# Performance work log

Hardware: AMD Instinct MI355X
Metric: run time of the kernel (lower is better)

## Reference

```python
import jax, jax.numpy as jnp
import numpy as np

N, E, G, S = 200000, 800000, 2048, 128
NUM_OPS, NUM_ETYPES, NUMERIC = 64, 4, 12
H, TEXT, VOCAB, OUT = 256, 64, 30000, 512
IN0 = 32 + NUMERIC  # 44


def _ln(h, eps=1e-5):
    # nn.LayerNorm with default (ones/zeros) affine, created fresh each forward
    m = h.mean(-1, keepdims=True)
    v = ((h - m) ** 2).mean(-1, keepdims=True)
    return (h - m) * jax.lax.rsqrt(v + eps)


def _leaky(v):
    return jnp.where(v > 0, v, 0.1 * v)  # LeakyReLU(0.1)


def setup_inputs() -> dict:
    key = jax.random.key(0)
    ks = jax.random.split(key, 40)
    x = jax.random.normal(ks[0], (N, 1 + NUMERIC), jnp.float32)
    x = x.at[:, 0].set(jax.random.randint(ks[1], (N,), 0, NUM_OPS).astype(jnp.float32))
    inp = {
        'x': x,
        'edge_index': jax.random.randint(ks[2], (2, E), 0, N),
        'edge_attr': jax.random.randint(ks[3], (E,), 0, NUM_ETYPES),
        'batch': jnp.sort(jax.random.randint(ks[4], (N,), 0, G)),
        'sql_ids': jax.random.randint(ks[5], (G, S), 0, VOCAB),
        'sql_mask': (jax.random.uniform(ks[6], (G, S)) > 0.3).astype(jnp.float32),
        'op_embed': jax.random.normal(ks[7], (NUM_OPS, 32), jnp.float32),
        'edge_embed': jax.random.normal(ks[8], (NUM_ETYPES, 16), jnp.float32),
        'token_embed': jax.random.normal(ks[9], (VOCAB, TEXT), jnp.float32).at[0].set(0.0),  # padding_idx=0
    }
    dims = [IN0, H, H]
    k = 10
    for i, d in enumerate(dims):
        inp[f'lin_w{i}'] = jax.random.normal(ks[k], (d, 16), jnp.float32) * 0.05; k += 1
        inp[f'lin_b{i}'] = jnp.zeros((d,), jnp.float32)
        inp[f'eps{i}'] = jnp.zeros((), jnp.float32)  # train_eps init 0
        inp[f'W1_{i}'] = jax.random.normal(ks[k], (H, d), jnp.float32) * 0.05; k += 1
        inp[f'b1_{i}'] = jnp.zeros((H,), jnp.float32)
        inp[f'W2_{i}'] = jax.random.normal(ks[k], (H, H), jnp.float32) * 0.05; k += 1
        inp[f'b2_{i}'] = jnp.zeros((H,), jnp.float32)
    inp['mW1'] = jax.random.normal(ks[k], (H, H + 3 + TEXT), jnp.float32) * 0.05; k += 1
    inp['mb1'] = jnp.zeros((H,), jnp.float32)
    inp['mW2'] = jax.random.normal(ks[k], (OUT, H), jnp.float32) * 0.05
    inp['mb2'] = jnp.zeros((OUT,), jnp.float32)
    return inp


def reference(x, edge_index, edge_attr, batch, sql_ids, sql_mask,
              op_embed, edge_embed, token_embed,
              lin_w0, lin_b0, eps0, W1_0, b1_0, W2_0, b2_0,
              lin_w1, lin_b1, eps1, W1_1, b1_1, W2_1, b2_1,
              lin_w2, lin_b2, eps2, W1_2, b1_2, W2_2, b2_2,
              mW1, mb1, mW2, mb2):
    op_ids = jnp.clip(x[:, 0].astype(jnp.int32), 0, NUM_OPS - 1)
    nums = x[:, 1:]
    e_idx = jnp.minimum(edge_attr, NUM_ETYPES - 1)  # clamp_max
    edge_emb = edge_embed[e_idx]                    # [E,16]
    h = jnp.concatenate([op_embed[op_ids], nums], 1)  # [N,44]
    src, dst = edge_index[0], edge_index[1]
    convs = [(lin_w0, lin_b0, eps0, W1_0, b1_0, W2_0, b2_0),
             (lin_w1, lin_b1, eps1, W1_1, b1_1, W2_1, b2_1),
             (lin_w2, lin_b2, eps2, W1_2, b1_2, W2_2, b2_2)]
    for (lw, lb, eps, W1, b1, W2, b2) in convs:
        h_in = h
        # GINEConv: msg = relu(x_j + Lin(edge_attr)); sum-aggregate at dst
        msg = jax.nn.relu(h[src] + edge_emb @ lw.T + lb)        # [E,d]
        aggr = jax.ops.segment_sum(msg, dst, num_segments=h.shape[0])
        z = (1.0 + eps) * h + aggr
        h = jax.nn.relu(z @ W1.T + b1) @ W2.T + b2              # conv MLP -> [N,H]
        h = _ln(h)
        h = _leaky(h + h_in) if h_in.shape[-1] == h.shape[-1] else _leaky(h)
    # graph pooling
    g = jax.ops.segment_sum(h, batch, num_segments=G)            # global_add_pool
    count = jax.ops.segment_sum(jnp.ones((h.shape[0],), h.dtype), batch, num_segments=G)
    denom = jnp.maximum(count, 1.0)                              # scatter_mean semantics
    fanout_mean = jax.ops.segment_sum(x[:, 5], batch, num_segments=G) / denom
    cost_mean = jax.ops.segment_sum(x[:, 4], batch, num_segments=G) / denom
    graph_sum = jnp.stack([count, fanout_mean, cost_mean], 1)    # [G,3]
    # text pooling (masked mean)
    emb = token_embed[sql_ids]                                   # [G,S,TEXT]
    summed = (emb * sql_mask[..., None]).sum(1)
    lengths = jnp.maximum(sql_mask.sum(1, keepdims=True), 1.0)
    text_feat = summed / lengths
    cat = jnp.concatenate([g, graph_sum, text_feat], 1)          # [G, H+3+TEXT]
    hid = _leaky(cat @ mW1.T + mb1)                              # Dropout(0.1) is identity in eval
    return hid @ mW2.T + mb2                                     # [G, OUT]
```

## Files before the change

kernel.cpp:

```cpp
#include <hip/hip_runtime.h>

#define NN 200000
#define EE 800000
#define GG 2048
#define NBLK ((NN + 255) / 256)

typedef __attribute__((ext_vector_type(8))) short short8;
typedef __attribute__((ext_vector_type(4))) float f32x4;

__device__ __forceinline__ float bf2f(ushort u){
  unsigned x = ((unsigned)u) << 16;
  return __uint_as_float(x);
}
__device__ __forceinline__ ushort f2bf(float f){
  unsigned x = __float_as_uint(f);
  x += 0x7fffu + ((x >> 16) & 1u);
  return (ushort)(x >> 16);
}

__device__ __forceinline__ void swz256(const float* __restrict__ W, ushort* __restrict__ o, int idx){
  int ks = idx >> 13, rem = idx & 8191;
  int j16 = rem >> 9, rem2 = rem & 511;
  int ln = rem2 >> 3, t = rem2 & 7;
  int row = j16*16 + (ln & 15);
  int k = ks*32 + (ln >> 4)*8 + t;
  o[idx] = f2bf(W[(size_t)row*256 + k]);
}

__global__ __launch_bounds__(256) void prep_k(
    const float* __restrict__ W10, const float* __restrict__ W20,
    const float* __restrict__ W11, const float* __restrict__ W21,
    const float* __restrict__ W12, const float* __restrict__ W22,
    const float* __restrict__ lw0, const float* __restrict__ lb0,
    const float* __restrict__ lw1, const float* __restrict__ lb1,
    const float* __restrict__ lw2, const float* __restrict__ lb2,
    const float* __restrict__ eE, const float* __restrict__ mW1,
    const float* __restrict__ mW2,
    ushort* __restrict__ wb10, ushort* __restrict__ wb20,
    ushort* __restrict__ wb11, ushort* __restrict__ wb21,
    ushort* __restrict__ wb12, ushort* __restrict__ wb22,
    ushort* __restrict__ mW1b, ushort* __restrict__ mW2b,
    float* __restrict__ eb)
{
  int b = blockIdx.x, tid = threadIdx.x;
  if (b < 64){
    int idx = b*256 + tid;
    int ks = idx >> 13, rem = idx & 8191;
    int j16 = rem >> 9, rem2 = rem & 511;
    int ln = rem2 >> 3, t = rem2 & 7;
    int row = j16*16 + (ln & 15);
    int k = ks*32 + (ln >> 4)*8 + t;
    wb10[idx] = (k < 44) ? f2bf(W10[row*44 + k]) : (ushort)0;
    return;
  }
  b -= 64;
  if (b < 256){ swz256(W20, wb20, b*256+tid); return; } b -= 256;
  if (b < 256){ swz256(W11, wb11, b*256+tid); return; } b -= 256;
  if (b < 256){ swz256(W21, wb21, b*256+tid); return; } b -= 256;
  if (b < 256){ swz256(W12, wb12, b*256+tid); return; } b -= 256;
  if (b < 256){ swz256(W22, wb22, b*256+tid); return; } b -= 256;
  if (b < 384){
    int idx = b*256 + tid; int o = idx / 384, k = idx - o*384;
    mW1b[idx] = (k < 323) ? f2bf(mW1[(size_t)o*323 + k]) : (ushort)0;
    return;
  }
  b -= 384;
  if (b < 512){ int idx = b*256+tid; mW2b[idx] = f2bf(mW2[idx]); return; } b -= 512;
  int li = b >> 2, t = b & 3;
  const float* lw = (li == 0) ? lw0 : ((li == 1) ? lw1 : lw2);
  const float* lb = (li == 0) ? lb0 : ((li == 1) ? lb1 : lb2);
  int d = (li == 0) ? 44 : 256;
  float v = 0.f;
  if (tid < d){
    float a = 0.f;
    #pragma unroll
    for (int j = 0; j < 16; j++) a += eE[t*16 + j] * lw[tid*16 + j];
    v = a + lb[tid];
  }
  eb[(li*4 + t)*256 + tid] = v;
}

__global__ __launch_bounds__(256) void build_h0_k(
    const float* __restrict__ x, const float* __restrict__ opE, ushort* __restrict__ h0)
{
  int idx = blockIdx.x*256 + threadIdx.x;
  int i = idx >> 6, c = idx & 63;
  float v = 0.f;
  if (c < 32){
    int op = (int)x[(size_t)i*13];
    op = op < 0 ? 0 : (op > 63 ? 63 : op);
    v = opE[op*32 + c];
  } else if (c < 44){
    v = x[(size_t)i*13 + (c - 31)];
  }
  h0[idx] = f2bf(v);
}

__global__ __launch_bounds__(256) void deg_k(const int* __restrict__ dst, int* __restrict__ D){
  int e = blockIdx.x*256 + threadIdx.x;
  atomicAdd(&D[dst[e]], 1);
}
__global__ __launch_bounds__(256) void scan1_k(int* __restrict__ D, int* __restrict__ bsum){
  __shared__ int s[256];
  int b = blockIdx.x, t = threadIdx.x, idx = b*256 + t;
  int v = (idx < NN) ? D[idx] : 0;
  s[t] = v; __syncthreads();
  for (int off = 1; off < 256; off <<= 1){
    int u = (t >= off) ? s[t-off] : 0;
    __syncthreads();
    s[t] += u;
    __syncthreads();
  }
  if (idx < NN) D[idx] = s[t] - v;
  if (t == 255) bsum[b] = s[255];
}
__global__ __launch_bounds__(256) void scan2_k(int* __restrict__ bsum){
  __shared__ int s[256];
  __shared__ int carry;
  int t = threadIdx.x;
  if (t == 0) carry = 0;
  __syncthreads();
  for (int c0 = 0; c0 < NBLK; c0 += 256){
    int idx = c0 + t;
    int v = (idx < NBLK) ? bsum[idx] : 0;
    s[t] = v; __syncthreads();
    for (int off = 1; off < 256; off <<= 1){
      int u = (t >= off) ? s[t-off] : 0;
      __syncthreads();
      s[t] += u;
      __syncthreads();
    }
    int ex = s[t] - v + carry;
    if (idx < NBLK) bsum[idx] = ex;
    int tot = s[255];
    __syncthreads();
    if (t == 0) carry += tot;
    __syncthreads();
  }
}
__global__ __launch_bounds__(256) void scan3_k(int* __restrict__ D, const int* __restrict__ bsum){
  int b = blockIdx.x, idx = b*256 + threadIdx.x;
  if (idx < NN) D[idx] += bsum[b];
}
__global__ __launch_bounds__(256) void fill_k(const int* __restrict__ src, const int* __restrict__ dst,
                                              const int* __restrict__ et, int* __restrict__ D,
                                              int* __restrict__ csr){
  int e = blockIdx.x*256 + threadIdx.x;
  int d = dst[e];
  int t = et[e]; t = t < 3 ? t : 3;
  int pos = atomicAdd(&D[d], 1);
  csr[pos] = src[e] | (t << 18);
}

template<int KD, int RESID>
__global__ __launch_bounds__(256) void layerf_k(
    const ushort* __restrict__ hsrc, const int* __restrict__ Dend, const int* __restrict__ csr,
    const float* __restrict__ ebL,
    const ushort* __restrict__ W1s, const float* __restrict__ b1,
    const ushort* __restrict__ W2s, const float* __restrict__ b2,
    const float* __restrict__ epsp, ushort* __restrict__ hout)
{
  __shared__ ushort ZT[32][264];
  __shared__ float ebs[1024];
  __shared__ float red1[32][4], red2[32][4], mnL[32], rsL[32];
  const int tid = threadIdx.x, lane = tid & 63, wv = tid >> 6;
  const int l15 = lane & 15, lq = lane >> 4;
  const int rowBase = blockIdx.x * 32;
  const float epv = 1.0f + epsp[0];
  const char* hb = (const char*)hsrc;

  if (KD == 256){
    for (int i = tid; i < 1024; i += 256) ebs[i] = ebL[i];
  } else {
    if (tid < 256) ebs[tid] = ebL[(tid >> 6)*256 + (tid & 63)];
  }
  __syncthreads();

  if (KD == 256){
    const int c = lane * 4;
    const unsigned c2 = lane * 8;
    #pragma unroll 1
    for (int it = 0; it < 2; it++){
      int rr0 = wv*8 + it*4;
      int r0 = rowBase + rr0;
      float4 A0, A1, A2, A3;
      {
        ushort4 q0 = *(const ushort4*)(hb + (size_t)(r0+0)*512 + c2);
        ushort4 q1 = *(const ushort4*)(hb + (size_t)(r0+1)*512 + c2);
        ushort4 q2 = *(const ushort4*)(hb + (size_t)(r0+2)*512 + c2);
        ushort4 q3 = *(const ushort4*)(hb + (size_t)(r0+3)*512 + c2);
        A0 = make_float4(epv*bf2f(q0.x), epv*bf2f(q0.y), epv*bf2f(q0.z), epv*bf2f(q0.w));
        A1 = make_float4(epv*bf2f(q1.x), epv*bf2f(q1.y), epv*bf2f(q1.z), epv*bf2f(q1.w));
        A2 = make_float4(epv*bf2f(q2.x), epv*bf2f(q2.y), epv*bf2f(q2.z), epv*bf2f(q2.w));
        A3 = make_float4(epv*bf2f(q3.x), epv*bf2f(q3.y), epv*bf2f(q3.z), epv*bf2f(q3.w));
      }
      int bm1 = (r0 == 0) ? 0 : Dend[r0-1];
      int e0 = Dend[r0], e1 = Dend[r0+1], e2 = Dend[r0+2], e3 = Dend[r0+3];
      int st0 = bm1, st1 = e0, st2 = e1, st3 = e2;
      int n0 = e0 - st0, n1 = e1 - st1, n2 = e2 - st2, n3 = e3 - st3;
      int nmax = n0 > n1 ? n0 : n1;
      nmax = nmax > n2 ? nmax : n2;
      nmax = nmax > n3 ? nmax : n3;
      ushort4 z4; z4.x = z4.y = z4.z = z4.w = 0;
      ushort4 sv0 = z4, sv1 = z4, sv2 = z4, sv3 = z4;
      int t0 = 0, t1 = 0, t2 = 0, t3 = 0;
      if (n0 > 0){ int p = csr[st0]; sv0 = *(const ushort4*)(hb + (unsigned)((p & 0x3FFFF) << 9) + c2); t0 = ((p >> 18) & 3)*256; }
      if (n1 > 0){ int p = csr[st1]; sv1 = *(const ushort4*)(hb + (unsigned)((p & 0x3FFFF) << 9) + c2); t1 = ((p >> 18) & 3)*256; }
      if (n2 > 0){ int p = csr[st2]; sv2 = *(const ushort4*)(hb + (unsigned)((p & 0x3FFFF) << 9) + c2); t2 = ((p >> 18) & 3)*256; }
      if (n3 > 0){ int p = csr[st3]; sv3 = *(const ushort4*)(hb + (unsigned)((p & 0x3FFFF) << 9) + c2); t3 = ((p >> 18) & 3)*256; }
      for (int k = 0; k < nmax; k++){
        ushort4 c0 = sv0, c1 = sv1, c2v = sv2, c3 = sv3;
        int u0 = t0, u1 = t1, u2 = t2, u3 = t3;
        if (k+1 < n0){ int p = csr[st0+k+1]; sv0 = *(const ushort4*)(hb + (unsigned)((p & 0x3FFFF) << 9) + c2); t0 = ((p >> 18) & 3)*256; }
        if (k+1 < n1){ int p = csr[st1+k+1]; sv1 = *(const ushort4*)(hb + (unsigned)((p & 0x3FFFF) << 9) + c2); t1 = ((p >> 18) & 3)*256; }
        if (k+1 < n2){ int p = csr[st2+k+1]; sv2 = *(const ushort4*)(hb + (unsigned)((p & 0x3FFFF) << 9) + c2); t2 = ((p >> 18) & 3)*256; }
        if (k+1 < n3){ int p = csr[st3+k+1]; sv3 = *(const ushort4*)(hb + (unsigned)((p & 0x3FFFF) << 9) + c2); t3 = ((p >> 18) & 3)*256; }
        if (k < n0){
          const float4 ev = *(const float4*)&ebs[u0 + c];
          float v;
          v = bf2f(c0.x) + ev.x; A0.x += v > 0.f ? v : 0.f;
          v = bf2f(c0.y) + ev.y; A0.y += v > 0.f ? v : 0.f;
          v = bf2f(c0.z) + ev.z; A0.z += v > 0.f ? v : 0.f;
          v = bf2f(c0.w) + ev.w; A0.w += v > 0.f ? v : 0.f;
        }
        if (k < n1){
          const float4 ev = *(const float4*)&ebs[u1 + c];
          float v;
          v = bf2f(c1.x) + ev.x; A1.x += v > 0.f ? v : 0.f;
          v = bf2f(c1.y) + ev.y; A1.y += v > 0.f ? v : 0.f;
          v = bf2f(c1.z) + ev.z; A1.z += v > 0.f ? v : 0.f;
          v = bf2f(c1.w) + ev.w; A1.w += v > 0.f ? v : 0.f;
        }
        if (k < n2){
          const float4 ev = *(const float4*)&ebs[u2 + c];
          float v;
          v = bf2f(c2v.x) + ev.x; A2.x += v > 0.f ? v : 0.f;
          v = bf2f(c2v.y) + ev.y; A2.y += v > 0.f ? v : 0.f;
          v = bf2f(c2v.z) + ev.z; A2.z += v > 0.f ? v : 0.f;
          v = bf2f(c2v.w) + ev.w; A2.w += v > 0.f ? v : 0.f;
        }
        if (k < n3){
          const float4 ev = *(const float4*)&ebs[u3 + c];
          float v;
          v = bf2f(c3.x) + ev.x; A3.x += v > 0.f ? v : 0.f;
          v = bf2f(c3.y) + ev.y; A3.y += v > 0.f ? v : 0.f;
          v = bf2f(c3.z) + ev.z; A3.z += v > 0.f ? v : 0.f;
          v = bf2f(c3.w) + ev.w; A3.w += v > 0.f ? v : 0.f;
        }
      }
      ushort4 o;
      o.x = f2bf(A0.x); o.y = f2bf(A0.y); o.z = f2bf(A0.z); o.w = f2bf(A0.w);
      *(ushort4*)&ZT[rr0+0][c] = o;
      o.x = f2bf(A1.x); o.y = f2bf(A1.y); o.z = f2bf(A1.z); o.w = f2bf(A1.w);
      *(ushort4*)&ZT[rr0+1][c] = o;
      o.x = f2bf(A2.x); o.y = f2bf(A2.y); o.z = f2bf(A2.z); o.w = f2bf(A2.w);
      *(ushort4*)&ZT[rr0+2][c] = o;
      o.x = f2bf(A3.x); o.y = f2bf(A3.y); o.z = f2bf(A3.z); o.w = f2bf(A3.w);
      *(ushort4*)&ZT[rr0+3][c] = o;
    }
  } else {
    const int c = l15 * 4;
    const unsigned c2 = l15 * 8;
    #pragma unroll 1
    for (int it = 0; it < 2; it++){
      int rr = wv*8 + it*4 + lq;
      int r = rowBase + rr;
      const ushort4 hv = *(const ushort4*)(hb + (size_t)r*128 + c2);
      float a0 = epv*bf2f(hv.x), a1 = epv*bf2f(hv.y), a2 = epv*bf2f(hv.z), a3 = epv*bf2f(hv.w);
      int st = (r == 0) ? 0 : Dend[r-1];
      int en = Dend[r];
      if (st < en){
        int p = csr[st];
        ushort4 sv = *(const ushort4*)(hb + (unsigned)((p & 0x3FFFF) << 7) + c2);
        int tt = ((p >> 18) & 3)*64;
        for (int e = st; e < en; e++){
          ushort4 cur = sv; int tc = tt;
          int e2 = (e+1 < en) ? e+1 : e;
          int p2 = csr[e2];
          sv = *(const ushort4*)(hb + (unsigned)((p2 & 0x3FFFF) << 7) + c2);
          tt = ((p2 >> 18) & 3)*64;
          const float4 ev = *(const float4*)&ebs[tc + c];
          float v;
          v = bf2f(cur.x) + ev.x; a0 += v > 0.f ? v : 0.f;
          v = bf2f(cur.y) + ev.y; a1 += v > 0.f ? v : 0.f;
          v = bf2f(cur.z) + ev.z; a2 += v > 0.f ? v : 0.f;
          v = bf2f(cur.w) + ev.w; a3 += v > 0.f ? v : 0.f;
        }
      }
      ushort4 o; o.x=f2bf(a0); o.y=f2bf(a1); o.z=f2bf(a2); o.w=f2bf(a3);
      *(ushort4*)&ZT[rr][c] = o;
    }
  }
  __syncthreads();

  f32x4 acc[2][4];
  #pragma unroll
  for (int i = 0; i < 2; i++)
    #pragma unroll
    for (int j = 0; j < 4; j++){ f32x4 z = {0.f,0.f,0.f,0.f}; acc[i][j] = z; }

  #pragma unroll
  for (int s = 0; s < KD/32; s++){
    short8 af[2], bfv[4];
    #pragma unroll
    for (int j = 0; j < 4; j++)
      bfv[j] = *(const short8*)(W1s + ((size_t)(s*16 + wv*4 + j)*64 + lane)*8);
    #pragma unroll
    for (int i = 0; i < 2; i++)
      af[i] = *(const short8*)&ZT[i*16 + l15][s*32 + lq*8];
    #pragma unroll
    for (int i = 0; i < 2; i++)
      #pragma unroll
      for (int j = 0; j < 4; j++)
        acc[i][j] = __builtin_amdgcn_mfma_f32_16x16x32_bf16(af[i], bfv[j], acc[i][j], 0, 0, 0);
  }
  __syncthreads();

  {
    float b1c[4];
    #pragma unroll
    for (int j = 0; j < 4; j++) b1c[j] = b1[wv*64 + j*16 + l15];
    #pragma unroll
    for (int i = 0; i < 2; i++)
      #pragma unroll
      for (int j = 0; j < 4; j++){
        int cc = wv*64 + j*16 + l15;
        #pragma unroll
        for (int rg = 0; rg < 4; rg++){
          int r = i*16 + (lq << 2) + rg;
          float v = acc[i][j][rg] + b1c[j];
          v = v > 0.f ? v : 0.f;
          ZT[r][cc] = f2bf(v);
        }
      }
  }
  __syncthreads();

  #pragma unroll
  for (int i = 0; i < 2; i++)
    #pragma unroll
    for (int j = 0; j < 4; j++){ f32x4 z = {0.f,0.f,0.f,0.f}; acc[i][j] = z; }

  #pragma unroll
  for (int s = 0; s < 8; s++){
    short8 af[2], bfv[4];
    #pragma unroll
    for (int j = 0; j < 4; j++)
      bfv[j] = *(const short8*)(W2s + ((size_t)(s*16 + wv*4 + j)*64 + lane)*8);
    #pragma unroll
    for (int i = 0; i < 2; i++)
      af[i] = *(const short8*)&ZT[i*16 + l15][s*32 + lq*8];
    #pragma unroll
    for (int i = 0; i < 2; i++)
      #pragma unroll
      for (int j = 0; j < 4; j++)
        acc[i][j] = __builtin_amdgcn_mfma_f32_16x16x32_bf16(af[i], bfv[j], acc[i][j], 0, 0, 0);
  }

  float b2c[4];
  #pragma unroll
  for (int j = 0; j < 4; j++) b2c[j] = b2[wv*64 + j*16 + l15];
  #pragma unroll
  for (int i = 0; i < 2; i++){
    #pragma unroll
    for (int rg = 0; rg < 4; rg++){
      float s1 = 0.f, s2 = 0.f;
      #pragma unroll
      for (int j = 0; j < 4; j++){
        float y = acc[i][j][rg] + b2c[j];
        s1 += y; s2 += y*y;
      }
      #pragma unroll
      for (int m = 1; m < 16; m <<= 1){
        s1 += __shfl_xor(s1, m, 64);
        s2 += __shfl_xor(s2, m, 64);
      }
      if (l15 == 0){
        int r = i*16 + (lq << 2) + rg;
        red1[r][wv] = s1; red2[r][wv] = s2;
      }
    }
  }
  __syncthreads();
  if (tid < 32){
    float s1 = red1[tid][0] + red1[tid][1] + red1[tid][2] + red1[tid][3];
    float s2 = red2[tid][0] + red2[tid][1] + red2[tid][2] + red2[tid][3];
    float mn = s1 * (1.f/256.f);
    float vr = s2 * (1.f/256.f) - mn*mn;
    mnL[tid] = mn;
    rsL[tid] = rsqrtf(vr + 1e-5f);
  }
  __syncthreads();
  #pragma unroll
  for (int i = 0; i < 2; i++){
    #pragma unroll
    for (int rg = 0; rg < 4; rg++){
      int r = i*16 + (lq << 2) + rg;
      float mn = mnL[r], rs = rsL[r];
      #pragma unroll
      for (int j = 0; j < 4; j++){
        int cc = wv*64 + j*16 + l15;
        float y = acc[i][j][rg] + b2c[j];
        float v = (y - mn) * rs;
        if (RESID) v += bf2f(hsrc[(size_t)(rowBase + r)*256 + cc]);
        v = v > 0.f ? v : 0.1f*v;
        ZT[r][cc] = f2bf(v);
      }
    }
  }
  __syncthreads();
  #pragma unroll
  for (int p = 0; p < 8; p++){
    int r = p*4 + (tid >> 6);
    int c = (tid & 63) * 4;
    *(ushort4*)(hout + (size_t)(rowBase + r)*256 + c) = *(const ushort4*)&ZT[r][c];
  }
}

__global__ __launch_bounds__(256) void readout_k(
    const ushort* __restrict__ h, const int* __restrict__ batch, const float* __restrict__ x,
    const int* __restrict__ sqlIds, const float* __restrict__ sqlMask,
    const float* __restrict__ tok, ushort* __restrict__ catb)
{
  int g = blockIdx.x, tid = threadIdx.x;
  const int lane = tid & 63, wv = tid >> 6;
  __shared__ int se[2];
  __shared__ float part[4][256];
  __shared__ float tpart[4][64];
  __shared__ float mpart[4];
  __shared__ float xs[2];
  if (tid < 2){
    int target = g + tid;
    int lo = 0, hi = NN;
    while (lo < hi){ int mid = (lo + hi) >> 1; if (batch[mid] < target) lo = mid + 1; else hi = mid; }
    se[tid] = lo;
  }
  __syncthreads();
  int start = se[0], end = se[1];
  {
    float a0 = 0.f, a1 = 0.f, a2 = 0.f, a3 = 0.f;
    for (int i = start + wv; i < end; i += 4){
      ushort4 q = *(const ushort4*)(h + (size_t)i*256 + lane*4);
      a0 += bf2f(q.x); a1 += bf2f(q.y); a2 += bf2f(q.z); a3 += bf2f(q.w);
    }
    part[wv][lane*4 + 0] = a0;
    part[wv][lane*4 + 1] = a1;
    part[wv][lane*4 + 2] = a2;
    part[wv][lane*4 + 3] = a3;
  }
  if (wv >= 2){
    int col = (wv == 2) ? 5 : 4;
    float s = 0.f;
    for (int i = start + lane; i < end; i += 64) s += x[(size_t)i*13 + col];
    #pragma unroll
    for (int m = 1; m < 64; m <<= 1) s += __shfl_xor(s, m, 64);
    if (lane == 0) xs[wv - 2] = s;
  }
  {
    int c = lane;
    float acc = 0.f, m = 0.f;
    for (int s = wv; s < 128; s += 4){
      int id = sqlIds[g*128 + s];
      float mk = sqlMask[g*128 + s];
      m += mk;
      acc += tok[(size_t)id*64 + c] * mk;
    }
    tpart[wv][c] = acc;
    if (c == 0) mpart[wv] = m;
  }
  __syncthreads();
  {
    float gsum = part[0][tid] + part[1][tid] + part[2][tid] + part[3][tid];
    catb[(size_t)g*384 + tid] = f2bf(gsum);
  }
  if (tid == 0){
    float cnt = (float)(end - start);
    float dn = cnt > 1.f ? cnt : 1.f;
    catb[(size_t)g*384 + 256] = f2bf(cnt);
    catb[(size_t)g*384 + 257] = f2bf(xs[0] / dn);
    catb[(size_t)g*384 + 258] = f2bf(xs[1] / dn);
  }
  if (tid < 64){
    float L = mpart[0] + mpart[1] + mpart[2] + mpart[3];
    L = L > 1.f ? L : 1.f;
    float tsum = tpart[0][tid] + tpart[1][tid] + tpart[2][tid] + tpart[3][tid];
    catb[(size_t)g*384 + 259 + tid] = f2bf(tsum / L);
  }
  if (tid >= 64 && tid < 125){
    catb[(size_t)g*384 + 259 + tid] = 0;
  }
}

__global__ __launch_bounds__(256) void head1_k(
    const ushort* __restrict__ catb, const ushort* __restrict__ W1b,
    const float* __restrict__ b1, ushort* __restrict__ hidb)
{
  __shared__ ushort smem[64*72 + 256*72];
  ushort (*As)[72] = (ushort(*)[72])smem;
  ushort (*Ws)[72] = (ushort(*)[72])(smem + 64*72);
  const int tid = threadIdx.x, lane = tid & 63, wv = tid >> 6;
  const int rowBase = blockIdx.x * 64;
  f32x4 acc[4][4];
  #pragma unroll
  for (int i = 0; i < 4; i++)
    #pragma unroll
    for (int j = 0; j < 4; j++){ f32x4 z = {0.f,0.f,0.f,0.f}; acc[i][j] = z; }

  for (int k0 = 0; k0 < 384; k0 += 64){
    __syncthreads();
    #pragma unroll
    for (int p = 0; p < 4; p++){
      int r = p*16 + (tid >> 4);
      int kk = (tid & 15) * 4;
      *(ushort4*)&As[r][kk] = *(const ushort4*)(catb + (size_t)(rowBase + r)*384 + k0 + kk);
    }
    #pragma unroll
    for (int p = 0; p < 16; p++){
      int oc = p*16 + (tid >> 4);
      int kk = (tid & 15) * 4;
      *(ushort4*)&Ws[oc][kk] = *(const ushort4*)(W1b + (size_t)oc*384 + k0 + kk);
    }
    __syncthreads();
    #pragma unroll
    for (int kc = 0; kc < 2; kc++){
      short8 af[4], bfv[4];
      #pragma unroll
      for (int i = 0; i < 4; i++)
        af[i] = *(const short8*)&As[i*16 + (lane & 15)][kc*32 + (lane >> 4)*8];
      #pragma unroll
      for (int j = 0; j < 4; j++)
        bfv[j] = *(const short8*)&Ws[wv*64 + j*16 + (lane & 15)][kc*32 + (lane >> 4)*8];
      #pragma unroll
      for (int i = 0; i < 4; i++)
        #pragma unroll
        for (int j = 0; j < 4; j++)
          acc[i][j] = __builtin_amdgcn_mfma_f32_16x16x32_bf16(af[i], bfv[j], acc[i][j], 0, 0, 0);
    }
  }
  __syncthreads();
  ushort (*Cs)[264] = (ushort(*)[264])smem;
  #pragma unroll
  for (int j = 0; j < 4; j++){
    int cc = wv*64 + j*16 + (lane & 15);
    float bb = b1[cc];
    #pragma unroll
    for (int i = 0; i < 4; i++){
      #pragma unroll
      for (int rg = 0; rg < 4; rg++){
        int r = i*16 + ((lane >> 4) << 2) + rg;
        float v = acc[i][j][rg] + bb;
        v = v > 0.f ? v : 0.1f*v;
        Cs[r][cc] = f2bf(v);
      }
    }
  }
  __syncthreads();
  #pragma unroll
  for (int p = 0; p < 16; p++){
    int r = p*4 + (tid >> 6);
    int c = (tid & 63) * 4;
    *(ushort4*)(hidb + (size_t)(rowBase + r)*256 + c) = *(const ushort4*)&Cs[r][c];
  }
}

__global__ __launch_bounds__(256) void head2_k(
    const ushort* __restrict__ hidb, const ushort* __restrict__ W2b,
    const float* __restrict__ b2, float* __restrict__ out)
{
  __shared__ float smemf[128*132];
  ushort (*As)[72] = (ushort(*)[72])smemf;
  ushort (*Bs)[72] = (ushort(*)[72])((ushort*)smemf + 128*72);
  const int tid = threadIdx.x, lane = tid & 63, wv = tid >> 6;
  const int wr = (wv >> 1) * 64;
  const int wc = (wv & 1) * 64;
  const int rowBase = blockIdx.x * 128;
  const int colBase = blockIdx.y * 128;
  const int lr = tid >> 4, lk = (tid & 15) * 4;

  f32x4 acc[4][4];
  #pragma unroll
  for (int i = 0; i < 4; i++)
    #pragma unroll
    for (int j = 0; j < 4; j++){ f32x4 z = {0.f,0.f,0.f,0.f}; acc[i][j] = z; }

  for (int k0 = 0; k0 < 256; k0 += 64){
    __syncthreads();
    #pragma unroll
    for (int p = 0; p < 8; p++){
      int r = lr + p*16;
      *(ushort4*)&As[r][lk] = *(const ushort4*)(hidb + (size_t)(rowBase + r)*256 + k0 + lk);
      *(ushort4*)&Bs[r][lk] = *(const ushort4*)(W2b + (size_t)(colBase + r)*256 + k0 + lk);
    }
    __syncthreads();
    #pragma unroll
    for (int kc = 0; kc < 2; kc++){
      short8 af[4], bfv[4];
      #pragma unroll
      for (int i = 0; i < 4; i++)
        af[i] = *(const short8*)&As[wr + i*16 + (lane & 15)][kc*32 + (lane >> 4)*8];
      #pragma unroll
      for (int j = 0; j < 4; j++)
        bfv[j] = *(const short8*)&Bs[wc + j*16 + (lane & 15)][kc*32 + (lane >> 4)*8];
      #pragma unroll
      for (int i = 0; i < 4; i++)
        #pragma unroll
        for (int j = 0; j < 4; j++)
          acc[i][j] = __builtin_amdgcn_mfma_f32_16x16x32_bf16(af[i], bfv[j], acc[i][j], 0, 0, 0);
    }
  }
  __syncthreads();
  float (*Cs)[132] = (float(*)[132])smemf;
  #pragma unroll
  for (int j = 0; j < 4; j++){
    int cl = wc + j*16 + (lane & 15);
    float bb = b2[colBase + cl];
    #pragma unroll
    for (int i = 0; i < 4; i++){
      int r0 = wr + i*16 + ((lane >> 4) << 2);
      #pragma unroll
      for (int rg = 0; rg < 4; rg++)
        Cs[r0 + rg][cl] = acc[i][j][rg] + bb;
    }
  }
  __syncthreads();
  #pragma unroll
  for (int p = 0; p < 16; p++){
    int r = (tid >> 5) + p*8;
    int c4 = (tid & 31) * 4;
    *(float4*)(out + (size_t)(rowBase + r)*512 + colBase + c4) = *(const float4*)&Cs[r][c4];
  }
}

extern "C" void kernel_launch(void* const* d_in, const int* in_sizes, int n_in,
                              void* d_out, int out_size, void* d_ws, size_t ws_size,
                              hipStream_t stream)
{
  const float* x       = (const float*)d_in[0];
  const int*   ei      = (const int*)d_in[1];
  const int*   src     = ei;
  const int*   dst     = ei + EE;
  const int*   eattr   = (const int*)d_in[2];
  const int*   batch   = (const int*)d_in[3];
  const int*   sqlIds  = (const int*)d_in[4];
  const float* sqlMask = (const float*)d_in[5];
  const float* opE     = (const float*)d_in[6];
  const float* eE      = (const float*)d_in[7];
  const float* tok     = (const float*)d_in[8];
  const float* lw0 = (const float*)d_in[9],  *lb0 = (const float*)d_in[10], *eps0 = (const float*)d_in[11];
  const float* W10 = (const float*)d_in[12], *b10 = (const float*)d_in[13];
  const float* W20 = (const float*)d_in[14], *b20 = (const float*)d_in[15];
  const float* lw1 = (const float*)d_in[16], *lb1 = (const float*)d_in[17], *eps1 = (const float*)d_in[18];
  const float* W11 = (const float*)d_in[19], *b11 = (const float*)d_in[20];
  const float* W21 = (const float*)d_in[21], *b21 = (const float*)d_in[22];
  const float* lw2 = (const float*)d_in[23], *lb2 = (const float*)d_in[24], *eps2 = (const float*)d_in[25];
  const float* W12 = (const float*)d_in[26], *b12 = (const float*)d_in[27];
  const float* W22 = (const float*)d_in[28], *b22 = (const float*)d_in[29];
  const float* mW1 = (const float*)d_in[30], *mb1 = (const float*)d_in[31];
  const float* mW2 = (const float*)d_in[32], *mb2 = (const float*)d_in[33];
  float* out = (float*)d_out;

  char* ws = (char*)d_ws;
  size_t off = 0;
  const size_t NB256 = (size_t)NN*256*2;
  ushort* bufH    = (ushort*)(ws + off); off += NB256;
  char*   region  = ws + off;            off += NB256;
  ushort* h0      = (ushort*)region;
  ushort* hPong   = (ushort*)region;
  ushort* catb    = (ushort*)region;
  ushort* hidb    = (ushort*)(region + (size_t)GG*384*2);
  ushort* wb10 = (ushort*)(ws + off); off += (size_t)256*64*2;
  ushort* wb20 = (ushort*)(ws + off); off += (size_t)65536*2;
  ushort* wb11 = (ushort*)(ws + off); off += (size_t)65536*2;
  ushort* wb21 = (ushort*)(ws + off); off += (size_t)65536*2;
  ushort* wb12 = (ushort*)(ws + off); off += (size_t)65536*2;
  ushort* wb22 = (ushort*)(ws + off); off += (size_t)65536*2;
  ushort* mW1b = (ushort*)(ws + off); off += (size_t)256*384*2;
  ushort* mW2b = (ushort*)(ws + off); off += (size_t)512*256*2;
  float*  eb   = (float*)(ws + off);  off += (size_t)3*4*256*4;
  int* D    = (int*)(ws + off); off += (size_t)NN*4;
  int* bsum = (int*)(ws + off); off += (size_t)NBLK*4;
  int* csr  = (int*)(ws + off); off += (size_t)EE*4;
  size_t needFast = off;

  if (ws_size < needFast) return;

  prep_k<<<2252, 256, 0, stream>>>(W10, W20, W11, W21, W12, W22,
                                   lw0, lb0, lw1, lb1, lw2, lb2, eE, mW1, mW2,
                                   wb10, wb20, wb11, wb21, wb12, wb22, mW1b, mW2b, eb);
  build_h0_k<<<50000, 256, 0, stream>>>(x, opE, h0);

  hipMemsetAsync(D, 0, (size_t)NN*4, stream);
  deg_k<<<3125, 256, 0, stream>>>(dst, D);
  scan1_k<<<NBLK, 256, 0, stream>>>(D, bsum);
  scan2_k<<<1, 256, 0, stream>>>(bsum);
  scan3_k<<<NBLK, 256, 0, stream>>>(D, bsum);
  fill_k<<<3125, 256, 0, stream>>>(src, dst, eattr, D, csr);

  layerf_k<64,0><<<6250, 256, 0, stream>>>(h0,    D, csr, eb,        wb10, b10, wb20, b20, eps0, bufH);
  layerf_k<256,1><<<6250, 256, 0, stream>>>(bufH, D, csr, eb + 1024, wb11, b11, wb21, b21, eps1, hPong);
  layerf_k<256,1><<<6250, 256, 0, stream>>>(hPong,D, csr, eb + 2048, wb12, b12, wb22, b22, eps2, bufH);

  readout_k<<<GG, 256, 0, stream>>>(bufH, batch, x, sqlIds, sqlMask, tok, catb);
  head1_k<<<32, 256, 0, stream>>>(catb, mW1b, mb1, hidb);
  head2_k<<<dim3(16, 4), 256, 0, stream>>>(hidb, mW2b, mb2, out);
}
```

Baseline: 835.7 us.

## Stream edges across eight rows per wave and XOR-swizzle the LDS tile

The KD=256 aggregation now has each wave walk one contiguous edge range covering its 8 destination rows. Four gathers stay in flight at all times, replacing the previous lockstep over 4 rows padded to the maximum degree. Row boundaries are handled by a flush that writes the finished row and starts the next one from prefetched self features. The ZT shared tile also changes from a padded 264-wide layout to an unpadded 256-wide layout with an XOR swizzle on 8-element chunks, to cut LDS use and avoid bank conflicts. The flush logic adds branchy control flow, and the swizzle adds address arithmetic to every LDS access.

Result: slower. 1.271 ms (+52.1%).

```diff
diff --git a/kernel.cpp b/kernel.cpp
--- a/kernel.cpp
+++ b/kernel.cpp
@@ -16,6 +16,9 @@
   unsigned x = __float_as_uint(f);
   x += 0x7fffu + ((x >> 16) & 1u);
   return (ushort)(x >> 16);
+}
+__device__ __forceinline__ int ztAddr(int r, int c){
+  return r*256 + (((c >> 3) ^ (r & 7)) << 3) + (c & 7);
 }
 
 __device__ __forceinline__ void swz256(const float* __restrict__ W, ushort* __restrict__ o, int idx){
@@ -160,7 +163,7 @@
     const ushort* __restrict__ W2s, const float* __restrict__ b2,
     const float* __restrict__ epsp, ushort* __restrict__ hout)
 {
-  __shared__ ushort ZT[32][264];
+  __shared__ ushort ZT[32*256];
   __shared__ float ebs[1024];
   __shared__ float red1[32][4], red2[32][4], mnL[32], rsL[32];
   const int tid = threadIdx.x, lane = tid & 63, wv = tid >> 6;
@@ -178,85 +181,75 @@
 
   if (KD == 256){
     const int c = lane * 4;
-    const unsigned c2 = lane * 8;
-    #pragma unroll 1
-    for (int it = 0; it < 2; it++){
-      int rr0 = wv*8 + it*4;
-      int r0 = rowBase + rr0;
-      float4 A0, A1, A2, A3;
+    const unsigned cb = lane * 8;
+    const int rBase8 = wv*8;
+    const int r0 = rowBase + rBase8;
+    const int end0 = Dend[r0+0], end1 = Dend[r0+1], end2 = Dend[r0+2], end3 = Dend[r0+3];
+    const int end4 = Dend[r0+4], end5 = Dend[r0+5], end6 = Dend[r0+6], end7 = Dend[r0+7];
+    int e = (r0 == 0) ? 0 : Dend[r0-1];
+    const int eEnd = end7;
+    int rr = 0;
+    int ebound = end0;
+    ushort4 hnext = *(const ushort4*)(hb + (size_t)(r0+1)*512 + cb);
+    int rowPf = 2;
+    float4 acc;
+    {
+      ushort4 hcur = *(const ushort4*)(hb + (size_t)r0*512 + cb);
+      acc = make_float4(epv*bf2f(hcur.x), epv*bf2f(hcur.y), epv*bf2f(hcur.z), epv*bf2f(hcur.w));
+    }
+    ushort4 sv0, sv1, sv2, sv3;
+    int t0 = 0, t1 = 0, t2 = 0, t3 = 0;
+    sv0.x=sv0.y=sv0.z=sv0.w=0; sv1=sv0; sv2=sv0; sv3=sv0;
+    if (e+0 < eEnd){ int p = csr[e+0]; sv0 = *(const ushort4*)(hb + (unsigned)((p & 0x3FFFF) << 9) + cb); t0 = ((p >> 18) & 3)*256; }
+    if (e+1 < eEnd){ int p = csr[e+1]; sv1 = *(const ushort4*)(hb + (unsigned)((p & 0x3FFFF) << 9) + cb); t1 = ((p >> 18) & 3)*256; }
+    if (e+2 < eEnd){ int p = csr[e+2]; sv2 = *(const ushort4*)(hb + (unsigned)((p & 0x3FFFF) << 9) + cb); t2 = ((p >> 18) & 3)*256; }
+    if (e+3 < eEnd){ int p = csr[e+3]; sv3 = *(const ushort4*)(hb + (unsigned)((p & 0x3FFFF) << 9) + cb); t3 = ((p >> 18) & 3)*256; }
+
+    auto flushTo = [&](int ee){
+      while (ee >= ebound){
+        ushort4 o; o.x = f2bf(acc.x); o.y = f2bf(acc.y); o.z = f2bf(acc.z); o.w = f2bf(acc.w);
+        *(ushort4*)(ZT + ztAddr(rBase8 + rr, c)) = o;
+        rr++;
+        acc = make_float4(epv*bf2f(hnext.x), epv*bf2f(hnext.y), epv*bf2f(hnext.z), epv*bf2f(hnext.w));
+        if (rowPf < 8){ hnext = *(const ushort4*)(hb + (size_t)(r0+rowPf)*512 + cb); rowPf++; }
+        ebound = (rr==1)?end1:(rr==2)?end2:(rr==3)?end3:(rr==4)?end4:(rr==5)?end5:(rr==6)?end6:end7;
+      }
+    };
+    auto consume = [&](const ushort4 s, int t){
+      const float4 ev = *(const float4*)&ebs[t + c];
+      float v;
+      v = bf2f(s.x) + ev.x; acc.x += v > 0.f ? v : 0.f;
+      v = bf2f(s.y) + ev.y; acc.y += v > 0.f ? v : 0.f;
+      v = bf2f(s.z) + ev.z; acc.z += v > 0.f ? v : 0.f;
+      v = bf2f(s.w) + ev.w; acc.w += v > 0.f ? v : 0.f;
+    };
+
+    for (int eb2 = e; eb2 < eEnd; eb2 += 4){
       {
-        ushort4 q0 = *(const ushort4*)(hb + (size_t)(r0+0)*512 + c2);
-        ushort4 q1 = *(const ushort4*)(hb + (size_t)(r0+1)*512 + c2);
-        ushort4 q2 = *(const ushort4*)(hb + (size_t)(r0+2)*512 + c2);
-        ushort4 q3 = *(const ushort4*)(hb + (size_t)(r0+3)*512 + c2);
-        A0 = make_float4(epv*bf2f(q0.x), epv*bf2f(q0.y), epv*bf2f(q0.z), epv*bf2f(q0.w));
-        A1 = make_float4(epv*bf2f(q1.x), epv*bf2f(q1.y), epv*bf2f(q1.z), epv*bf2f(q1.w));
-        A2 = make_float4(epv*bf2f(q2.x), epv*bf2f(q2.y), epv*bf2f(q2.z), epv*bf2f(q2.w));
-        A3 = make_float4(epv*bf2f(q3.x), epv*bf2f(q3.y), epv*bf2f(q3.z), epv*bf2f(q3.w));
-      }
-      int bm1 = (r0 == 0) ? 0 : Dend[r0-1];
-      int e0 = Dend[r0], e1 = Dend[r0+1], e2 = Dend[r0+2], e3 = Dend[r0+3];
-      int st0 = bm1, st1 = e0, st2 = e1, st3 = e2;
-      int n0 = e0 - st0, n1 = e1 - st1, n2 = e2 - st2, n3 = e3 - st3;
-      int nmax = n0 > n1 ? n0 : n1;
-      nmax = nmax > n2 ? nmax : n2;
-      nmax = nmax > n3 ? nmax : n3;
-      ushort4 z4; z4.x = z4.y = z4.z = z4.w = 0;
-      ushort4 sv0 = z4, sv1 = z4, sv2 = z4, sv3 = z4;
-      int t0 = 0, t1 = 0, t2 = 0, t3 = 0;
-      if (n0 > 0){ int p = csr[st0]; sv0 = *(const ushort4*)(hb + (unsigned)((p & 0x3FFFF) << 9) + c2); t0 = ((p >> 18) & 3)*256; }
-      if (n1 > 0){ int p = csr[st1]; sv1 = *(const ushort4*)(hb + (unsigned)((p & 0x3FFFF) << 9) + c2); t1 = ((p >> 18) & 3)*256; }
-      if (n2 > 0){ int p = csr[st2]; sv2 = *(const ushort4*)(hb + (unsigned)((p & 0x3FFFF) << 9) + c2); t2 = ((p >> 18) & 3)*256; }
-      if (n3 > 0){ int p = csr[st3]; sv3 = *(const ushort4*)(hb + (unsigned)((p & 0x3FFFF) << 9) + c2); t3 = ((p >> 18) & 3)*256; }
-      for (int k = 0; k < nmax; k++){
-        ushort4 c0 = sv0, c1 = sv1, c2v = sv2, c3 = sv3;
-        int u0 = t0, u1 = t1, u2 = t2, u3 = t3;
-        if (k+1 < n0){ int p = csr[st0+k+1]; sv0 = *(const ushort4*)(hb + (unsigned)((p & 0x3FFFF) << 9) + c2); t0 = ((p >> 18) & 3)*256; }
-        if (k+1 < n1){ int p = csr[st1+k+1]; sv1 = *(const ushort4*)(hb + (unsigned)((p & 0x3FFFF) << 9) + c2); t1 = ((p >> 18) & 3)*256; }
-        if (k+1 < n2){ int p = csr[st2+k+1]; sv2 = *(const ushort4*)(hb + (unsigned)((p & 0x3FFFF) << 9) + c2); t2 = ((p >> 18) & 3)*256; }
-        if (k+1 < n3){ int p = csr[st3+k+1]; sv3 = *(const ushort4*)(hb + (unsigned)((p & 0x3FFFF) << 9) + c2); t3 = ((p >> 18) & 3)*256; }
-        if (k < n0){
-          const float4 ev = *(const float4*)&ebs[u0 + c];
-          float v;
-          v = bf2f(c0.x) + ev.x; A0.x += v > 0.f ? v : 0.f;
-          v = bf2f(c0.y) + ev.y; A0.y += v > 0.f ? v : 0.f;
-          v = bf2f(c0.z) + ev.z; A0.z += v > 0.f ? v : 0.f;
-          v = bf2f(c0.w) + ev.w; A0.w += v > 0.f ? v : 0.f;
-        }
-        if (k < n1){
-          const float4 ev = *(const float4*)&ebs[u1 + c];
-          float v;
-          v = bf2f(c1.x) + ev.x; A1.x += v > 0.f ? v : 0.f;
-          v = bf2f(c1.y) + ev.y; A1.y += v > 0.f ? v : 0.f;
-          v = bf2f(c1.z) + ev.z; A1.z += v > 0.f ? v : 0.f;
-          v = bf2f(c1.w) + ev.w; A1.w += v > 0.f ? v : 0.f;
-        }
-        if (k < n2){
-          const float4 ev = *(const float4*)&ebs[u2 + c];
-          float v;
-          v = bf2f(c2v.x) + ev.x; A2.x += v > 0.f ? v : 0.f;
-          v = bf2f(c2v.y) + ev.y; A2.y += v > 0.f ? v : 0.f;
-          v = bf2f(c2v.z) + ev.z; A2.z += v > 0.f ? v : 0.f;
-          v = bf2f(c2v.w) + ev.w; A2.w += v > 0.f ? v : 0.f;
-        }
-        if (k < n3){
-          const float4 ev = *(const float4*)&ebs[u3 + c];
-          float v;
-          v = bf2f(c3.x) + ev.x; A3.x += v > 0.f ? v : 0.f;
-          v = bf2f(c3.y) + ev.y; A3.y += v > 0.f ? v : 0.f;
-          v = bf2f(c3.z) + ev.z; A3.z += v > 0.f ? v : 0.f;
-          v = bf2f(c3.w) + ev.w; A3.w += v > 0.f ? v : 0.f;
-        }
-      }
-      ushort4 o;
-      o.x = f2bf(A0.x); o.y = f2bf(A0.y); o.z = f2bf(A0.z); o.w = f2bf(A0.w);
-      *(ushort4*)&ZT[rr0+0][c] = o;
-      o.x = f2bf(A1.x); o.y = f2bf(A1.y); o.z = f2bf(A1.z); o.w = f2bf(A1.w);
-      *(ushort4*)&ZT[rr0+1][c] = o;
-      o.x = f2bf(A2.x); o.y = f2bf(A2.y); o.z = f2bf(A2.z); o.w = f2bf(A2.w);
-      *(ushort4*)&ZT[rr0+2][c] = o;
-      o.x = f2bf(A3.x); o.y = f2bf(A3.y); o.z = f2bf(A3.z); o.w = f2bf(A3.w);
-      *(ushort4*)&ZT[rr0+3][c] = o;
+        int ee = eb2;
+        flushTo(ee); consume(sv0, t0);
+        if (ee+4 < eEnd){ int p = csr[ee+4]; sv0 = *(const ushort4*)(hb + (unsigned)((p & 0x3FFFF) << 9) + cb); t0 = ((p >> 18) & 3)*256; }
+      }
+      { int ee = eb2+1; if (ee < eEnd){
+          flushTo(ee); consume(sv1, t1);
+          if (ee+4 < eEnd){ int p = csr[ee+4]; sv1 = *(const ushort4*)(hb + (unsigned)((p & 0x3FFFF) << 9) + cb); t1 = ((p >> 18) & 3)*256; }
+      } }
+      { int ee = eb2+2; if (ee < eEnd){
+          flushTo(ee); consume(sv2, t2);
+          if (ee+4 < eEnd){ int p = csr[ee+4]; sv2 = *(const ushort4*)(hb + (unsigned)((p & 0x3FFFF) << 9) + cb); t2 = ((p >> 18) & 3)*256; }
+      } }
+      { int ee = eb2+3; if (ee < eEnd){
+          flushTo(ee); consume(sv3, t3);
+          if (ee+4 < eEnd){ int p = csr[ee+4]; sv3 = *(const ushort4*)(hb + (unsigned)((p & 0x3FFFF) << 9) + cb); t3 = ((p >> 18) & 3)*256; }
+      } }
+    }
+    for (;;){
+      ushort4 o; o.x = f2bf(acc.x); o.y = f2bf(acc.y); o.z = f2bf(acc.z); o.w = f2bf(acc.w);
+      *(ushort4*)(ZT + ztAddr(rBase8 + rr, c)) = o;
+      if (rr == 7) break;
+      rr++;
+      acc = make_float4(epv*bf2f(hnext.x), epv*bf2f(hnext.y), epv*bf2f(hnext.z), epv*bf2f(hnext.w));
+      if (rowPf < 8){ hnext = *(const ushort4*)(hb + (size_t)(r0+rowPf)*512 + cb); rowPf++; }
     }
   } else {
     const int c = l15 * 4;
@@ -288,7 +281,7 @@
         }
       }
       ushort4 o; o.x=f2bf(a0); o.y=f2bf(a1); o.z=f2bf(a2); o.w=f2bf(a3);
-      *(ushort4*)&ZT[rr][c] = o;
+      *(ushort4*)(ZT + ztAddr(rr, c)) = o;
     }
   }
   __syncthreads();
@@ -306,8 +299,10 @@
     for (int j = 0; j < 4; j++)
       bfv[j] = *(const short8*)(W1s + ((size_t)(s*16 + wv*4 + j)*64 + lane)*8);
     #pragma unroll
-    for (int i = 0; i < 2; i++)
-      af[i] = *(const short8*)&ZT[i*16 + l15][s*32 + lq*8];
+    for (int i = 0; i < 2; i++){
+      int row = i*16 + l15;
+      af[i] = *(const short8*)(ZT + row*256 + (((s*4 + lq) ^ (l15 & 7)) << 3));
+    }
     #pragma unroll
     for (int i = 0; i < 2; i++)
       #pragma unroll
@@ -330,7 +325,7 @@
           int r = i*16 + (lq << 2) + rg;
           float v = acc[i][j][rg] + b1c[j];
           v = v > 0.f ? v : 0.f;
-          ZT[r][cc] = f2bf(v);
+          ZT[ztAddr(r, cc)] = f2bf(v);
         }
       }
   }
@@ -348,8 +343,10 @@
     for (int j = 0; j < 4; j++)
       bfv[j] = *(const short8*)(W2s + ((size_t)(s*16 + wv*4 + j)*64 + lane)*8);
     #pragma unroll
-    for (int i = 0; i < 2; i++)
-      af[i] = *(const short8*)&ZT[i*16 + l15][s*32 + lq*8];
+    for (int i = 0; i < 2; i++){
+      int row = i*16 + l15;
+      af[i] = *(const short8*)(ZT + row*256 + (((s*4 + lq) ^ (l15 & 7)) << 3));
+    }
     #pragma unroll
     for (int i = 0; i < 2; i++)
       #pragma unroll
@@ -404,7 +401,7 @@
         float v = (y - mn) * rs;
         if (RESID) v += bf2f(hsrc[(size_t)(rowBase + r)*256 + cc]);
         v = v > 0.f ? v : 0.1f*v;
-        ZT[r][cc] = f2bf(v);
+        ZT[ztAddr(r, cc)] = f2bf(v);
       }
     }
   }
@@ -413,7 +410,7 @@
   for (int p = 0; p < 8; p++){
     int r = p*4 + (tid >> 6);
     int c = (tid & 63) * 4;
-    *(ushort4*)(hout + (size_t)(rowBase + r)*256 + c) = *(const ushort4*)&ZT[r][c];
+    *(ushort4*)(hout + (size_t)(rowBase + r)*256 + c) = *(const ushort4*)(ZT + ztAddr(r, c));
   }
 }
 
```
